# Performance work log

Measured on AMD Instinct MI355X. Metric: run time of the kernel, lower is better.

## Reference

```python
import jax, jax.numpy as jnp
import numpy as np

N_NODES = 50000
N_EDGES = 600000
DIM = 128
N_LAYERS = 5


def setup_inputs() -> dict:
    key = jax.random.key(0)
    k1, k2, k3, k4 = jax.random.split(key, 4)
    x = jax.random.normal(k1, (N_NODES, DIM), dtype=jnp.float32)
    edge_index = jax.random.randint(k2, (2, N_EDGES), 0, N_NODES, dtype=jnp.int64)
    # small init scale to keep 5-layer activations numerically sane
    W_l = jax.random.normal(k3, (N_LAYERS, DIM, DIM), dtype=jnp.float32) * 0.05
    W_r = jax.random.normal(k4, (N_LAYERS, DIM, DIM), dtype=jnp.float32) * 0.05
    b_l = jnp.zeros((N_LAYERS, DIM), dtype=jnp.float32)
    return {"x": x, "edge_index": edge_index, "W_l": W_l, "b_l": b_l, "W_r": W_r}


def reference(x, edge_index, W_l, b_l, W_r):
    """GraphSAGE forward: 5 stacked SAGEConv (mean aggr) + relu between layers.
    Dropout is identity (eval mode). SAGEConv: out = lin_l(mean_j x_j) + lin_r(x_i).
    """
    src = edge_index[0]  # message sources (x_j)
    dst = edge_index[1]  # aggregation targets (x_i)
    n = x.shape[0]
    # in-degree for mean aggregation (clamped to avoid div-by-zero)
    deg = jax.ops.segment_sum(jnp.ones_like(dst, dtype=x.dtype), dst, num_segments=n)
    inv_deg = 1.0 / jnp.maximum(deg, 1.0)  # [N]
    n_layers = W_l.shape[0]
    for i in range(n_layers):
        msg = x[src]  # [E, D] gather
        aggr = jax.ops.segment_sum(msg, dst, num_segments=n) * inv_deg[:, None]  # [N, D]
        x = aggr @ W_l[i] + b_l[i] + x @ W_r[i]
        if i < n_layers - 1:
            x = jax.nn.relu(x)
    return x
```

## Files before the change

### kernel.cpp

```cpp
#include <hip/hip_runtime.h>

#define NDIM 128

typedef __attribute__((ext_vector_type(8))) short s16x8;
typedef __attribute__((ext_vector_type(4))) float f32x4;

__device__ __forceinline__ unsigned short f2bf(float f) {
    unsigned u = __float_as_uint(f);
    u += 0x7FFFu + ((u >> 16) & 1u);
    return (unsigned short)(u >> 16);
}
__device__ __forceinline__ float bf2f(unsigned short h) {
    return __uint_as_float((unsigned)h << 16);
}
__device__ __forceinline__ unsigned short f2h(float f) {
    _Float16 h = (_Float16)f;
    return *(unsigned short*)&h;
}

__device__ __forceinline__ void g2lds16(const void* g, void* l) {
    __builtin_amdgcn_global_load_lds(
        (const __attribute__((address_space(1))) void*)g,
        (__attribute__((address_space(3))) void*)l, 16, 0, 0);
}

__global__ __launch_bounds__(256) void detect_kernel(
    const int* __restrict__ raw, int* __restrict__ flag, int E) {
    __shared__ int any_nz;
    if (threadIdx.x == 0) any_nz = 0;
    __syncthreads();
    int local = 0;
    const int samples = (E < 4096) ? E : 4096;
#pragma unroll
    for (int j = 0; j < 16; ++j) {
        int i = threadIdx.x * 16 + j;
        if (i < samples) local |= raw[2 * i + 1];
    }
    if (local) atomicOr(&any_nz, 1);
    __syncthreads();
    if (threadIdx.x == 0) *flag = any_nz;
}

__global__ void convert_kernel(const int* __restrict__ raw, const int* __restrict__ flag,
                               int* __restrict__ idx, int* __restrict__ deg, int E) {
    int i = blockIdx.x * 256 + threadIdx.x;
    if (i >= 2 * E) return;
    int v = (*flag == 0) ? raw[2 * i] : raw[i];
    idx[i] = v;
    if (i >= E) atomicAdd(&deg[v], 1);
}

__global__ __launch_bounds__(256) void deg_reduce_kernel(
    const int* __restrict__ deg, int* __restrict__ partials, int n) {
    const int base = blockIdx.x * 1024;
    const int tid = threadIdx.x;
    int s = 0;
#pragma unroll
    for (int j = 0; j < 4; ++j) {
        int i = base + tid * 4 + j;
        if (i < n) s += deg[i];
    }
#pragma unroll
    for (int off = 32; off; off >>= 1) s += __shfl_down(s, off);
    __shared__ int ws[4];
    if ((tid & 63) == 0) ws[tid >> 6] = s;
    __syncthreads();
    if (tid == 0) partials[blockIdx.x] = ws[0] + ws[1] + ws[2] + ws[3];
}

__global__ void scan_partials_kernel(int* __restrict__ partials, int nb,
                                     int* __restrict__ row_start, int n) {
    __shared__ int sh[1024];
    const int tid = threadIdx.x;
    int v = (tid < nb) ? partials[tid] : 0;
    sh[tid] = v;
    __syncthreads();
    for (int off = 1; off < 1024; off <<= 1) {
        int a = sh[tid];
        int b = (tid >= off) ? sh[tid - off] : 0;
        __syncthreads();
        sh[tid] = a + b;
        __syncthreads();
    }
    if (tid < nb) partials[tid] = (tid == 0) ? 0 : sh[tid - 1];
    if (tid == 0) row_start[n] = sh[1023];
}

__global__ __launch_bounds__(256) void deg_downsweep_kernel(
    const int* __restrict__ deg, const int* __restrict__ partials,
    int* __restrict__ row_start, int* __restrict__ cursor,
    float* __restrict__ inv_deg, int n) {
    const int base = blockIdx.x * 1024;
    const int tid = threadIdx.x;
    const int i0 = base + tid * 4;
    int d[4];
    int s = 0;
#pragma unroll
    for (int j = 0; j < 4; ++j) {
        int i = i0 + j;
        d[j] = (i < n) ? deg[i] : 0;
        s += d[j];
    }
    const int lane = tid & 63;
    int incl = s;
#pragma unroll
    for (int off = 1; off < 64; off <<= 1) {
        int t = __shfl_up(incl, off);
        if (lane >= off) incl += t;
    }
    __shared__ int wsum[4];
    if (lane == 63) wsum[tid >> 6] = incl;
    __syncthreads();
    int woff = 0;
    const int w = tid >> 6;
    for (int k = 0; k < w; ++k) woff += wsum[k];
    int excl = incl - s + woff + partials[blockIdx.x];
#pragma unroll
    for (int j = 0; j < 4; ++j) {
        int i = i0 + j;
        if (i < n) {
            row_start[i] = excl;
            cursor[i] = excl;
            inv_deg[i] = 1.0f / (float)max(d[j], 1);
            excl += d[j];
        }
    }
}

__global__ __launch_bounds__(256) void scatter_kernel(
    const int* __restrict__ idx, int* __restrict__ cursor,
    int* __restrict__ sorted_src, int E) {
    const int i0 = (blockIdx.x * 256 + threadIdx.x) * 4;
    if (i0 >= E) return;
    int s[4], d[4], p[4];
#pragma unroll
    for (int j = 0; j < 4; ++j) {
        if (i0 + j < E) {
            s[j] = idx[i0 + j];
            d[j] = idx[E + i0 + j];
        }
    }
#pragma unroll
    for (int j = 0; j < 4; ++j)
        if (i0 + j < E) p[j] = atomicAdd(&cursor[d[j]], 1);
#pragma unroll
    for (int j = 0; j < 4; ++j)
        if (i0 + j < E) sorted_src[p[j]] = s[j];
}

__global__ __launch_bounds__(256) void presplit_kernel(
    const float* __restrict__ Wl, const float* __restrict__ Wr,
    short* __restrict__ wfrag, int total) {
    int idx = blockIdx.x * 256 + threadIdx.x;
    if (idx >= total) return;
    int j = idx & 7;
    int lane = (idx >> 3) & 63;
    int ct = (idx >> 9) & 7;
    int chunk = (idx >> 12) & 3;
    int plane = (idx >> 14) & 3;
    int l = idx >> 16;
    int nn = ct * 16 + (lane & 15);
    int k = chunk * 32 + (lane >> 4) * 8 + j;
    const float* src = (plane < 2) ? Wl : Wr;
    float v = src[(size_t)l * 16384 + (size_t)k * 128 + nn];
    unsigned short h = f2bf(v);
    wfrag[idx] = (plane & 1) ? (short)f2bf(v - bf2f(h)) : (short)h;
}

__global__ __launch_bounds__(256) void split_x_kernel(
    const float* __restrict__ X, short* __restrict__ Xbf,
    short* __restrict__ Xf16, int total4) {
    int i = blockIdx.x * 256 + threadIdx.x;
    if (i >= total4) return;
    float4 v = *(const float4*)(X + (size_t)i * 4);
    float vv[4] = {v.x, v.y, v.z, v.w};
    unsigned short h[4], lo[4], f[4];
#pragma unroll
    for (int m = 0; m < 4; ++m) {
        h[m] = f2bf(vv[m]);
        lo[m] = f2bf(vv[m] - bf2f(h[m]));
        f[m] = f2h(vv[m]);
    }
    const int node = i >> 5;
    const int u = (i & 31) * 4;
    *(int2*)(Xbf + (size_t)node * 256 + u) = make_int2(
        (int)(h[0] | ((unsigned)h[1] << 16)), (int)(h[2] | ((unsigned)h[3] << 16)));
    *(int2*)(Xbf + (size_t)node * 256 + 128 + u) = make_int2(
        (int)(lo[0] | ((unsigned)lo[1] << 16)), (int)(lo[2] | ((unsigned)lo[3] << 16)));
    *(int2*)(Xf16 + (size_t)node * 128 + u) = make_int2(
        (int)(f[0] | ((unsigned)f[1] << 16)), (int)(f[2] | ((unsigned)f[3] << 16)));
}

__global__ __launch_bounds__(256) void aggregate_kernel(
    const short* __restrict__ Xf16, const int* __restrict__ row_start,
    const int* __restrict__ sorted_src, const float* __restrict__ inv_deg,
    short* __restrict__ Agbf, int n) {
    int gid = blockIdx.x * 256 + threadIdx.x;
    int node = gid >> 5;
    if (node >= n) return;
    const int lane32 = threadIdx.x & 31;
    const int q = lane32 << 2;
    const int beg = row_start[node];
    const int end = row_start[node + 1];
    float4 acc = make_float4(0.f, 0.f, 0.f, 0.f);
    for (int base = beg; base < end; base += 32) {
        const int cnt = min(end - base, 32);
        const int my_src = (lane32 < cnt) ? sorted_src[base + lane32] : 0;
        for (int jb = 0; jb < cnt; jb += 8) {
            int2 v[8];
            float m[8];
#pragma unroll
            for (int t = 0; t < 8; ++t) {
                const int j = jb + t;
                const int js = (j < cnt) ? j : (cnt - 1);
                const int s = __shfl(my_src, js, 32);
                v[t] = *(const int2*)(Xf16 + (size_t)s * 128 + q);
                m[t] = (j < cnt) ? 1.f : 0.f;
            }
#pragma unroll
            for (int t = 0; t < 8; ++t) {
                union { int2 i2; _Float16 h[4]; } u;
                u.i2 = v[t];
                acc.x = fmaf(m[t], (float)u.h[0], acc.x);
                acc.y = fmaf(m[t], (float)u.h[1], acc.y);
                acc.z = fmaf(m[t], (float)u.h[2], acc.z);
                acc.w = fmaf(m[t], (float)u.h[3], acc.w);
            }
        }
    }
    const float inv = inv_deg[node];
    acc.x *= inv; acc.y *= inv; acc.z *= inv; acc.w *= inv;
    float vv[4] = {acc.x, acc.y, acc.z, acc.w};
    unsigned short h[4], lo[4];
#pragma unroll
    for (int m = 0; m < 4; ++m) {
        h[m] = f2bf(vv[m]);
        lo[m] = f2bf(vv[m] - bf2f(h[m]));
    }
    *(int2*)(Agbf + (size_t)node * 256 + q) = make_int2(
        (int)(h[0] | ((unsigned)h[1] << 16)), (int)(h[2] | ((unsigned)h[3] << 16)));
    *(int2*)(Agbf + (size_t)node * 256 + 128 + q) = make_int2(
        (int)(lo[0] | ((unsigned)lo[1] << 16)), (int)(lo[2] | ((unsigned)lo[3] << 16)));
}

__global__ __launch_bounds__(256, 4) void gemm_kernel(
    const short* __restrict__ Agbf, const short* __restrict__ Xbf,
    const short* __restrict__ wfrag,
    const float* __restrict__ bias,
    float* __restrict__ Yf, short* __restrict__ Ybf, short* __restrict__ Yf16,
    int n, int do_relu) {
    __shared__ __align__(16) short sT[4][64][64];
    const int tid = threadIdx.x;
    const int lane = tid & 63;
    const int wave = tid >> 6;
    const int ln15 = lane & 15;
    const int quad = lane >> 4;
    const int row0 = blockIdx.x * 64;
    const int wr0 = (wave & 1) * 32;
    const int wc0 = (wave >> 1) * 64;
    const int ctbase = (wave >> 1) * 4;

    f32x4 acc[2][4];
#pragma unroll
    for (int i = 0; i < 2; ++i)
#pragma unroll
        for (int j = 0; j < 4; ++j) acc[i][j] = (f32x4)(0.f);

    const short* pbase = (wave < 2) ? Agbf : Xbf;
    const int plo = (wave & 1) * 128;
    const int rl = lane >> 3;
    const int gslot = (lane & 7) ^ rl;

    for (int kp = 0; kp < 2; ++kp) {
        __syncthreads();
#pragma unroll
        for (int i = 0; i < 8; ++i) {
            int grow = row0 + i * 8 + rl;
            if (grow >= n) grow = n - 1;
            const short* g = pbase + (size_t)grow * 256 + plo + kp * 64 + gslot * 8;
            g2lds16(g, &sT[wave][i * 8][0]);
        }
        __syncthreads();

#pragma unroll
        for (int ch = 0; ch < 2; ++ch) {
            const int chunk = kp * 2 + ch;
            s16x8 fAgh[2], fAgl[2], fXh[2], fXl[2];
#pragma unroll
            for (int rt = 0; rt < 2; ++rt) {
                const int r = wr0 + rt * 16 + ln15;
                const int cc = (ch * 4 + quad) ^ (r & 7);
                fAgh[rt] = *(const s16x8*)&sT[0][r][cc * 8];
                fAgl[rt] = *(const s16x8*)&sT[1][r][cc * 8];
                fXh[rt]  = *(const s16x8*)&sT[2][r][cc * 8];
                fXl[rt]  = *(const s16x8*)&sT[3][r][cc * 8];
            }
#pragma unroll
            for (int ct = 0; ct < 4; ++ct) {
                const short* wb = wfrag + (chunk << 12) + ((ctbase + ct) << 9) + (lane << 3);
                const s16x8 blh = *(const s16x8*)(wb);
                const s16x8 bll = *(const s16x8*)(wb + 16384);
                const s16x8 brh = *(const s16x8*)(wb + 32768);
                const s16x8 brl = *(const s16x8*)(wb + 49152);
#pragma unroll
                for (int rt = 0; rt < 2; ++rt) {
                    acc[rt][ct] = __builtin_amdgcn_mfma_f32_16x16x32_bf16(fAgh[rt], blh, acc[rt][ct], 0, 0, 0);
                    acc[rt][ct] = __builtin_amdgcn_mfma_f32_16x16x32_bf16(fAgh[rt], bll, acc[rt][ct], 0, 0, 0);
                    acc[rt][ct] = __builtin_amdgcn_mfma_f32_16x16x32_bf16(fAgl[rt], blh, acc[rt][ct], 0, 0, 0);
                    acc[rt][ct] = __builtin_amdgcn_mfma_f32_16x16x32_bf16(fXh[rt],  brh, acc[rt][ct], 0, 0, 0);
                    acc[rt][ct] = __builtin_amdgcn_mfma_f32_16x16x32_bf16(fXh[rt],  brl, acc[rt][ct], 0, 0, 0);
                    acc[rt][ct] = __builtin_amdgcn_mfma_f32_16x16x32_bf16(fXl[rt],  brh, acc[rt][ct], 0, 0, 0);
                }
            }
        }
    }

#pragma unroll
    for (int rt = 0; rt < 2; ++rt) {
#pragma unroll
        for (int ct = 0; ct < 4; ++ct) {
            const int col = wc0 + ct * 16 + ln15;
            const float bv = bias[col];
#pragma unroll
            for (int r = 0; r < 4; ++r) {
                const int grow = row0 + wr0 + rt * 16 + quad * 4 + r;
                if (grow < n) {
                    float v = acc[rt][ct][r] + bv;
                    if (do_relu) v = fmaxf(v, 0.f);
                    if (Yf) {
                        Yf[(size_t)grow * NDIM + col] = v;
                    } else {
                        unsigned short h = f2bf(v);
                        Ybf[(size_t)grow * 256 + col] = (short)h;
                        Ybf[(size_t)grow * 256 + 128 + col] = (short)f2bf(v - bf2f(h));
                        Yf16[(size_t)grow * 128 + col] = (short)f2h(v);
                    }
                }
            }
        }
    }
}

extern "C" void kernel_launch(void* const* d_in, const int* in_sizes, int n_in,
                              void* d_out, int out_size, void* d_ws, size_t ws_size,
                              hipStream_t stream) {
    const float* x0   = (const float*)d_in[0];
    const int*   eraw = (const int*)d_in[1];
    const float* Wl   = (const float*)d_in[2];
    const float* bl   = (const float*)d_in[3];
    const float* Wr   = (const float*)d_in[4];
    float* out = (float*)d_out;

    const int N = in_sizes[0] / NDIM;
    const int E = in_sizes[1] / 2;

    auto align_up = [](size_t v) { return (v + 255) & ~(size_t)255; };
    char* p = (char*)d_ws;
    int* idx = (int*)p;                 p += align_up((size_t)2 * E * 4);
    int* deg = (int*)p;                 p += align_up((size_t)(N + 1) * 4);
    int* flag = deg + N;
    int* row_start = (int*)p;           p += align_up((size_t)(N + 1) * 4);
    int* cursor = (int*)p;              p += align_up((size_t)N * 4);
    int* ssrc = (int*)p;                p += align_up((size_t)E * 4);
    float* invd = (float*)p;            p += align_up((size_t)N * 4);
    int* partials = (int*)p;            p += align_up((size_t)1024 * 4);
    short* wfrag = (short*)p;           p += align_up((size_t)327680 * 2);
    short* bf[3];
    for (int s = 0; s < 3; ++s) {
        bf[s] = (short*)p;              p += align_up((size_t)N * 256 * 2);
    }
    short* f16[2];
    for (int s = 0; s < 2; ++s) {
        f16[s] = (short*)p;             p += align_up((size_t)N * 128 * 2);
    }

    const int nb = (N + 1023) / 1024;

    hipMemsetAsync(deg, 0, (size_t)N * 4, stream);
    detect_kernel<<<1, 256, 0, stream>>>(eraw, flag, E);
    convert_kernel<<<(2 * E + 255) / 256, 256, 0, stream>>>(eraw, flag, idx, deg, E);
    deg_reduce_kernel<<<nb, 256, 0, stream>>>(deg, partials, N);
    scan_partials_kernel<<<1, 1024, 0, stream>>>(partials, nb, row_start, N);
    deg_downsweep_kernel<<<nb, 256, 0, stream>>>(deg, partials, row_start, cursor, invd, N);
    scatter_kernel<<<(E + 1023) / 1024, 256, 0, stream>>>(idx, cursor, ssrc, E);
    presplit_kernel<<<1280, 256, 0, stream>>>(Wl, Wr, wfrag, 327680);
    split_x_kernel<<<(N * 32 + 255) / 256, 256, 0, stream>>>(x0, bf[0], f16[0], N * 32);

    int xs = 0, fp = 0;
    for (int l = 0; l < 5; ++l) {
        const int as_ = (xs + 1) % 3;
        const int ys = (xs + 2) % 3;
        aggregate_kernel<<<(N * 32 + 255) / 256, 256, 0, stream>>>(
            f16[fp], row_start, ssrc, invd, bf[as_], N);
        if (l < 4) {
            gemm_kernel<<<(N + 63) / 64, 256, 0, stream>>>(
                bf[as_], bf[xs], wfrag + (size_t)l * 65536,
                bl + (size_t)l * NDIM, nullptr, bf[ys], f16[fp ^ 1], N, 1);
        } else {
            gemm_kernel<<<(N + 63) / 64, 256, 0, stream>>>(
                bf[as_], bf[xs], wfrag + (size_t)l * 65536,
                bl + (size_t)l * NDIM, out, nullptr, nullptr, N, 0);
        }
        xs = ys;
        fp ^= 1;
    }
}
```

Before: 424.1 us.

## Stage only aggregated operand in LDS, load X fragments directly from global

The GEMM kernel now copies the whole 64-row aggregated-feature tile (hi and lo halves) into LDS in one pass, using a new swizzle, behind a single barrier. The X operand fragments are read straight from global memory into registers instead of going through LDS. This removes the two-phase staging loop and its extra barriers, trading them for uncoalesced-ish direct global reads of X, which are duplicated across the two column-half waves.

```diff
diff --git a/kernel.cpp b/kernel.cpp
--- a/kernel.cpp
+++ b/kernel.cpp
@@ -249,7 +249,7 @@
     const float* __restrict__ bias,
     float* __restrict__ Yf, short* __restrict__ Ybf, short* __restrict__ Yf16,
     int n, int do_relu) {
-    __shared__ __align__(16) short sT[4][64][64];
+    __shared__ __align__(16) short sAg[64][256];
     const int tid = threadIdx.x;
     const int lane = tid & 63;
     const int wave = tid >> 6;
@@ -260,57 +260,64 @@
     const int wc0 = (wave >> 1) * 64;
     const int ctbase = (wave >> 1) * 4;
 
+    {
+        const int rl = lane >> 5;
+        const int c = lane & 31;
+#pragma unroll
+        for (int i = 0; i < 8; ++i) {
+            const int rloc = wave * 16 + i * 2 + rl;
+            int grow = row0 + rloc;
+            if (grow >= n) grow = n - 1;
+            const int sslot = (c & 24) | ((c ^ rloc) & 7);
+            const short* g = Agbf + (size_t)grow * 256 + sslot * 8;
+            g2lds16(g, &sAg[wave * 16 + i * 2][0]);
+        }
+    }
+
     f32x4 acc[2][4];
 #pragma unroll
     for (int i = 0; i < 2; ++i)
 #pragma unroll
         for (int j = 0; j < 4; ++j) acc[i][j] = (f32x4)(0.f);
 
-    const short* pbase = (wave < 2) ? Agbf : Xbf;
-    const int plo = (wave & 1) * 128;
-    const int rl = lane >> 3;
-    const int gslot = (lane & 7) ^ rl;
-
-    for (int kp = 0; kp < 2; ++kp) {
-        __syncthreads();
-#pragma unroll
-        for (int i = 0; i < 8; ++i) {
-            int grow = row0 + i * 8 + rl;
-            if (grow >= n) grow = n - 1;
-            const short* g = pbase + (size_t)grow * 256 + plo + kp * 64 + gslot * 8;
-            g2lds16(g, &sT[wave][i * 8][0]);
-        }
-        __syncthreads();
-
-#pragma unroll
-        for (int ch = 0; ch < 2; ++ch) {
-            const int chunk = kp * 2 + ch;
-            s16x8 fAgh[2], fAgl[2], fXh[2], fXl[2];
+    const short* xrow[2];
+#pragma unroll
+    for (int rt = 0; rt < 2; ++rt) {
+        int grow = row0 + wr0 + rt * 16 + ln15;
+        if (grow >= n) grow = n - 1;
+        xrow[rt] = Xbf + (size_t)grow * 256;
+    }
+
+    __syncthreads();
+
+#pragma unroll
+    for (int chunk = 0; chunk < 4; ++chunk) {
+        const int u = chunk * 4 + quad;
+        s16x8 fAgh[2], fAgl[2], fXh[2], fXl[2];
+#pragma unroll
+        for (int rt = 0; rt < 2; ++rt) {
+            const int r = wr0 + rt * 16 + ln15;
+            const int sh_ = (u & 24) | ((u ^ r) & 7);
+            fAgh[rt] = *(const s16x8*)&sAg[r][sh_ * 8];
+            fAgl[rt] = *(const s16x8*)&sAg[r][(sh_ + 16) * 8];
+            fXh[rt]  = *(const s16x8*)(xrow[rt] + u * 8);
+            fXl[rt]  = *(const s16x8*)(xrow[rt] + 128 + u * 8);
+        }
+#pragma unroll
+        for (int ct = 0; ct < 4; ++ct) {
+            const short* wb = wfrag + (chunk << 12) + ((ctbase + ct) << 9) + (lane << 3);
+            const s16x8 blh = *(const s16x8*)(wb);
+            const s16x8 bll = *(const s16x8*)(wb + 16384);
+            const s16x8 brh = *(const s16x8*)(wb + 32768);
+            const s16x8 brl = *(const s16x8*)(wb + 49152);
 #pragma unroll
             for (int rt = 0; rt < 2; ++rt) {
-                const int r = wr0 + rt * 16 + ln15;
-                const int cc = (ch * 4 + quad) ^ (r & 7);
-                fAgh[rt] = *(const s16x8*)&sT[0][r][cc * 8];
-                fAgl[rt] = *(const s16x8*)&sT[1][r][cc * 8];
-                fXh[rt]  = *(const s16x8*)&sT[2][r][cc * 8];
-                fXl[rt]  = *(const s16x8*)&sT[3][r][cc * 8];
-            }
-#pragma unroll
-            for (int ct = 0; ct < 4; ++ct) {
-                const short* wb = wfrag + (chunk << 12) + ((ctbase + ct) << 9) + (lane << 3);
-                const s16x8 blh = *(const s16x8*)(wb);
-                const s16x8 bll = *(const s16x8*)(wb + 16384);
-                const s16x8 brh = *(const s16x8*)(wb + 32768);
-                const s16x8 brl = *(const s16x8*)(wb + 49152);
-#pragma unroll
-                for (int rt = 0; rt < 2; ++rt) {
-                    acc[rt][ct] = __builtin_amdgcn_mfma_f32_16x16x32_bf16(fAgh[rt], blh, acc[rt][ct], 0, 0, 0);
-                    acc[rt][ct] = __builtin_amdgcn_mfma_f32_16x16x32_bf16(fAgh[rt], bll, acc[rt][ct], 0, 0, 0);
-                    acc[rt][ct] = __builtin_amdgcn_mfma_f32_16x16x32_bf16(fAgl[rt], blh, acc[rt][ct], 0, 0, 0);
-                    acc[rt][ct] = __builtin_amdgcn_mfma_f32_16x16x32_bf16(fXh[rt],  brh, acc[rt][ct], 0, 0, 0);
-                    acc[rt][ct] = __builtin_amdgcn_mfma_f32_16x16x32_bf16(fXh[rt],  brl, acc[rt][ct], 0, 0, 0);
-                    acc[rt][ct] = __builtin_amdgcn_mfma_f32_16x16x32_bf16(fXl[rt],  brh, acc[rt][ct], 0, 0, 0);
-                }
+                acc[rt][ct] = __builtin_amdgcn_mfma_f32_16x16x32_bf16(fAgh[rt], blh, acc[rt][ct], 0, 0, 0);
+                acc[rt][ct] = __builtin_amdgcn_mfma_f32_16x16x32_bf16(fAgh[rt], bll, acc[rt][ct], 0, 0, 0);
+                acc[rt][ct] = __builtin_amdgcn_mfma_f32_16x16x32_bf16(fAgl[rt], blh, acc[rt][ct], 0, 0, 0);
+                acc[rt][ct] = __builtin_amdgcn_mfma_f32_16x16x32_bf16(fXh[rt],  brh, acc[rt][ct], 0, 0, 0);
+                acc[rt][ct] = __builtin_amdgcn_mfma_f32_16x16x32_bf16(fXh[rt],  brl, acc[rt][ct], 0, 0, 0);
+                acc[rt][ct] = __builtin_amdgcn_mfma_f32_16x16x32_bf16(fXl[rt],  brh, acc[rt][ct], 0, 0, 0);
             }
         }
     }
```

Result: slower. 440.9 us (+4.0%).

## Switch activations to single fp16 and weights to scaled fp16 hi/lo split

Applied to the files above, without the earlier changes.

Replaces the bf16 hi/lo split representation of activations and aggregates with a single fp16 copy. Weights become fp16 hi plus a residual scaled by 2048 and kept in a separate accumulator. This halves activation bytes read and written by the GEMM and aggregate kernels, cuts the MFMA count per tile from 6 to 4, and halves LDS staging. The cost is lower precision on activations (fp16 only, no low part) and a risk of fp16 range overflow.

```diff
diff --git a/kernel.cpp b/kernel.cpp
--- a/kernel.cpp
+++ b/kernel.cpp
@@ -3,19 +3,16 @@
 #define NDIM 128
 
 typedef __attribute__((ext_vector_type(8))) short s16x8;
+typedef __attribute__((ext_vector_type(8))) _Float16 h16x8;
 typedef __attribute__((ext_vector_type(4))) float f32x4;
 
-__device__ __forceinline__ unsigned short f2bf(float f) {
-    unsigned u = __float_as_uint(f);
-    u += 0x7FFFu + ((u >> 16) & 1u);
-    return (unsigned short)(u >> 16);
-}
-__device__ __forceinline__ float bf2f(unsigned short h) {
-    return __uint_as_float((unsigned)h << 16);
-}
 __device__ __forceinline__ unsigned short f2h(float f) {
     _Float16 h = (_Float16)f;
     return *(unsigned short*)&h;
+}
+__device__ __forceinline__ float h2f(unsigned short u) {
+    _Float16 h = *(_Float16*)&u;
+    return (float)h;
 }
 
 __device__ __forceinline__ void g2lds16(const void* g, void* l) {
@@ -163,38 +160,27 @@
     int k = chunk * 32 + (lane >> 4) * 8 + j;
     const float* src = (plane < 2) ? Wl : Wr;
     float v = src[(size_t)l * 16384 + (size_t)k * 128 + nn];
-    unsigned short h = f2bf(v);
-    wfrag[idx] = (plane & 1) ? (short)f2bf(v - bf2f(h)) : (short)h;
+    unsigned short h = f2h(v);
+    wfrag[idx] = (plane & 1) ? (short)f2h((v - h2f(h)) * 2048.0f) : (short)h;
 }
 
 __global__ __launch_bounds__(256) void split_x_kernel(
-    const float* __restrict__ X, short* __restrict__ Xbf,
-    short* __restrict__ Xf16, int total4) {
+    const float* __restrict__ X, short* __restrict__ Xf16, int total4) {
     int i = blockIdx.x * 256 + threadIdx.x;
     if (i >= total4) return;
     float4 v = *(const float4*)(X + (size_t)i * 4);
     float vv[4] = {v.x, v.y, v.z, v.w};
-    unsigned short h[4], lo[4], f[4];
-#pragma unroll
-    for (int m = 0; m < 4; ++m) {
-        h[m] = f2bf(vv[m]);
-        lo[m] = f2bf(vv[m] - bf2f(h[m]));
-        f[m] = f2h(vv[m]);
-    }
-    const int node = i >> 5;
-    const int u = (i & 31) * 4;
-    *(int2*)(Xbf + (size_t)node * 256 + u) = make_int2(
-        (int)(h[0] | ((unsigned)h[1] << 16)), (int)(h[2] | ((unsigned)h[3] << 16)));
-    *(int2*)(Xbf + (size_t)node * 256 + 128 + u) = make_int2(
-        (int)(lo[0] | ((unsigned)lo[1] << 16)), (int)(lo[2] | ((unsigned)lo[3] << 16)));
-    *(int2*)(Xf16 + (size_t)node * 128 + u) = make_int2(
+    unsigned short f[4];
+#pragma unroll
+    for (int m = 0; m < 4; ++m) f[m] = f2h(vv[m]);
+    *(int2*)(Xf16 + (size_t)i * 4) = make_int2(
         (int)(f[0] | ((unsigned)f[1] << 16)), (int)(f[2] | ((unsigned)f[3] << 16)));
 }
 
 __global__ __launch_bounds__(256) void aggregate_kernel(
     const short* __restrict__ Xf16, const int* __restrict__ row_start,
     const int* __restrict__ sorted_src, const float* __restrict__ inv_deg,
-    short* __restrict__ Agbf, int n) {
+    short* __restrict__ Agf16, int n) {
     int gid = blockIdx.x * 256 + threadIdx.x;
     int node = gid >> 5;
     if (node >= n) return;
@@ -230,26 +216,18 @@
     }
     const float inv = inv_deg[node];
     acc.x *= inv; acc.y *= inv; acc.z *= inv; acc.w *= inv;
-    float vv[4] = {acc.x, acc.y, acc.z, acc.w};
-    unsigned short h[4], lo[4];
-#pragma unroll
-    for (int m = 0; m < 4; ++m) {
-        h[m] = f2bf(vv[m]);
-        lo[m] = f2bf(vv[m] - bf2f(h[m]));
-    }
-    *(int2*)(Agbf + (size_t)node * 256 + q) = make_int2(
-        (int)(h[0] | ((unsigned)h[1] << 16)), (int)(h[2] | ((unsigned)h[3] << 16)));
-    *(int2*)(Agbf + (size_t)node * 256 + 128 + q) = make_int2(
-        (int)(lo[0] | ((unsigned)lo[1] << 16)), (int)(lo[2] | ((unsigned)lo[3] << 16)));
+    unsigned short f[4] = {f2h(acc.x), f2h(acc.y), f2h(acc.z), f2h(acc.w)};
+    *(int2*)(Agf16 + (size_t)node * 128 + q) = make_int2(
+        (int)(f[0] | ((unsigned)f[1] << 16)), (int)(f[2] | ((unsigned)f[3] << 16)));
 }
 
 __global__ __launch_bounds__(256, 4) void gemm_kernel(
-    const short* __restrict__ Agbf, const short* __restrict__ Xbf,
+    const short* __restrict__ Agf16, const short* __restrict__ Xf16,
     const short* __restrict__ wfrag,
     const float* __restrict__ bias,
-    float* __restrict__ Yf, short* __restrict__ Ybf, short* __restrict__ Yf16,
+    float* __restrict__ Yf, short* __restrict__ Yf16,
     int n, int do_relu) {
-    __shared__ __align__(16) short sT[4][64][64];
+    __shared__ __align__(16) short sT[2][64][64];
     const int tid = threadIdx.x;
     const int lane = tid & 63;
     const int wave = tid >> 6;
@@ -260,56 +238,53 @@
     const int wc0 = (wave >> 1) * 64;
     const int ctbase = (wave >> 1) * 4;
 
-    f32x4 acc[2][4];
+    f32x4 accM[2][4], accR[2][4];
 #pragma unroll
     for (int i = 0; i < 2; ++i)
 #pragma unroll
-        for (int j = 0; j < 4; ++j) acc[i][j] = (f32x4)(0.f);
-
-    const short* pbase = (wave < 2) ? Agbf : Xbf;
-    const int plo = (wave & 1) * 128;
+        for (int j = 0; j < 4; ++j) { accM[i][j] = (f32x4)(0.f); accR[i][j] = (f32x4)(0.f); }
+
+    const short* pbase = (wave < 2) ? Agf16 : Xf16;
+    const int rhalf = (wave & 1) * 32;
     const int rl = lane >> 3;
     const int gslot = (lane & 7) ^ rl;
 
     for (int kp = 0; kp < 2; ++kp) {
         __syncthreads();
 #pragma unroll
-        for (int i = 0; i < 8; ++i) {
-            int grow = row0 + i * 8 + rl;
+        for (int i = 0; i < 4; ++i) {
+            const int rloc = rhalf + i * 8;
+            int grow = row0 + rloc + rl;
             if (grow >= n) grow = n - 1;
-            const short* g = pbase + (size_t)grow * 256 + plo + kp * 64 + gslot * 8;
-            g2lds16(g, &sT[wave][i * 8][0]);
+            const short* g = pbase + (size_t)grow * 128 + kp * 64 + gslot * 8;
+            g2lds16(g, &sT[wave >> 1][rloc][0]);
         }
         __syncthreads();
 
 #pragma unroll
         for (int ch = 0; ch < 2; ++ch) {
             const int chunk = kp * 2 + ch;
-            s16x8 fAgh[2], fAgl[2], fXh[2], fXl[2];
+            h16x8 fAg[2], fX[2];
 #pragma unroll
             for (int rt = 0; rt < 2; ++rt) {
                 const int r = wr0 + rt * 16 + ln15;
                 const int cc = (ch * 4 + quad) ^ (r & 7);
-                fAgh[rt] = *(const s16x8*)&sT[0][r][cc * 8];
-                fAgl[rt] = *(const s16x8*)&sT[1][r][cc * 8];
-                fXh[rt]  = *(const s16x8*)&sT[2][r][cc * 8];
-                fXl[rt]  = *(const s16x8*)&sT[3][r][cc * 8];
+                fAg[rt] = *(const h16x8*)&sT[0][r][cc * 8];
+                fX[rt]  = *(const h16x8*)&sT[1][r][cc * 8];
             }
 #pragma unroll
             for (int ct = 0; ct < 4; ++ct) {
                 const short* wb = wfrag + (chunk << 12) + ((ctbase + ct) << 9) + (lane << 3);
-                const s16x8 blh = *(const s16x8*)(wb);
-                const s16x8 bll = *(const s16x8*)(wb + 16384);
-                const s16x8 brh = *(const s16x8*)(wb + 32768);
-                const s16x8 brl = *(const s16x8*)(wb + 49152);
+                const h16x8 wlh = *(const h16x8*)(wb);
+                const h16x8 wll = *(const h16x8*)(wb + 16384);
+                const h16x8 wrh = *(const h16x8*)(wb + 32768);
+                const h16x8 wrl = *(const h16x8*)(wb + 49152);
 #pragma unroll
                 for (int rt = 0; rt < 2; ++rt) {
-                    acc[rt][ct] = __builtin_amdgcn_mfma_f32_16x16x32_bf16(fAgh[rt], blh, acc[rt][ct], 0, 0, 0);
-                    acc[rt][ct] = __builtin_amdgcn_mfma_f32_16x16x32_bf16(fAgh[rt], bll, acc[rt][ct], 0, 0, 0);
-                    acc[rt][ct] = __builtin_amdgcn_mfma_f32_16x16x32_bf16(fAgl[rt], blh, acc[rt][ct], 0, 0, 0);
-                    acc[rt][ct] = __builtin_amdgcn_mfma_f32_16x16x32_bf16(fXh[rt],  brh, acc[rt][ct], 0, 0, 0);
-                    acc[rt][ct] = __builtin_amdgcn_mfma_f32_16x16x32_bf16(fXh[rt],  brl, acc[rt][ct], 0, 0, 0);
-                    acc[rt][ct] = __builtin_amdgcn_mfma_f32_16x16x32_bf16(fXl[rt],  brh, acc[rt][ct], 0, 0, 0);
+                    accM[rt][ct] = __builtin_amdgcn_mfma_f32_16x16x32_f16(fAg[rt], wlh, accM[rt][ct], 0, 0, 0);
+                    accR[rt][ct] = __builtin_amdgcn_mfma_f32_16x16x32_f16(fAg[rt], wll, accR[rt][ct], 0, 0, 0);
+                    accM[rt][ct] = __builtin_amdgcn_mfma_f32_16x16x32_f16(fX[rt],  wrh, accM[rt][ct], 0, 0, 0);
+                    accR[rt][ct] = __builtin_amdgcn_mfma_f32_16x16x32_f16(fX[rt],  wrl, accR[rt][ct], 0, 0, 0);
                 }
             }
         }
@@ -325,14 +300,11 @@
             for (int r = 0; r < 4; ++r) {
                 const int grow = row0 + wr0 + rt * 16 + quad * 4 + r;
                 if (grow < n) {
-                    float v = acc[rt][ct][r] + bv;
+                    float v = accM[rt][ct][r] + accR[rt][ct][r] * 4.8828125e-4f + bv;
                     if (do_relu) v = fmaxf(v, 0.f);
                     if (Yf) {
                         Yf[(size_t)grow * NDIM + col] = v;
                     } else {
-                        unsigned short h = f2bf(v);
-                        Ybf[(size_t)grow * 256 + col] = (short)h;
-                        Ybf[(size_t)grow * 256 + 128 + col] = (short)f2bf(v - bf2f(h));
                         Yf16[(size_t)grow * 128 + col] = (short)f2h(v);
                     }
                 }
@@ -365,12 +337,8 @@
     float* invd = (float*)p;            p += align_up((size_t)N * 4);
     int* partials = (int*)p;            p += align_up((size_t)1024 * 4);
     short* wfrag = (short*)p;           p += align_up((size_t)327680 * 2);
-    short* bf[3];
+    short* f16[3];
     for (int s = 0; s < 3; ++s) {
-        bf[s] = (short*)p;              p += align_up((size_t)N * 256 * 2);
-    }
-    short* f16[2];
-    for (int s = 0; s < 2; ++s) {
         f16[s] = (short*)p;             p += align_up((size_t)N * 128 * 2);
     }
 
@@ -384,24 +352,23 @@
     deg_downsweep_kernel<<<nb, 256, 0, stream>>>(deg, partials, row_start, cursor, invd, N);
     scatter_kernel<<<(E + 1023) / 1024, 256, 0, stream>>>(idx, cursor, ssrc, E);
     presplit_kernel<<<1280, 256, 0, stream>>>(Wl, Wr, wfrag, 327680);
-    split_x_kernel<<<(N * 32 + 255) / 256, 256, 0, stream>>>(x0, bf[0], f16[0], N * 32);
-
-    int xs = 0, fp = 0;
+    split_x_kernel<<<(N * 32 + 255) / 256, 256, 0, stream>>>(x0, f16[0], N * 32);
+
+    int xs = 0;
     for (int l = 0; l < 5; ++l) {
         const int as_ = (xs + 1) % 3;
         const int ys = (xs + 2) % 3;
         aggregate_kernel<<<(N * 32 + 255) / 256, 256, 0, stream>>>(
-            f16[fp], row_start, ssrc, invd, bf[as_], N);
+            f16[xs], row_start, ssrc, invd, f16[as_], N);
         if (l < 4) {
             gemm_kernel<<<(N + 63) / 64, 256, 0, stream>>>(
-                bf[as_], bf[xs], wfrag + (size_t)l * 65536,
-                bl + (size_t)l * NDIM, nullptr, bf[ys], f16[fp ^ 1], N, 1);
+                f16[as_], f16[xs], wfrag + (size_t)l * 65536,
+                bl + (size_t)l * NDIM, nullptr, f16[ys], N, 1);
         } else {
             gemm_kernel<<<(N + 63) / 64, 256, 0, stream>>>(
-                bf[as_], bf[xs], wfrag + (size_t)l * 65536,
-                bl + (size_t)l * NDIM, out, nullptr, nullptr, N, 0);
+                f16[as_], f16[xs], wfrag + (size_t)l * 65536,
+                bl + (size_t)l * NDIM, out, nullptr, N, 0);
         }
         xs = ys;
-        fp ^= 1;
-    }
-}
+    }
+}
```

Measured after the change: 357.5 us. 15.7% less time.
